# Optimization experiments

Measured on AMD Instinct MI355X. Metric: run time of the kernel, lower is better.

Reference implementation:

```python
import jax, jax.numpy as jnp
import numpy as np

B, S, E, F, C, V = 4, 2048, 100, 64, 8922, 52000

def _conv1d_same(x, w, b, k):
    # x: [B,E,S], w: [F,E,k] -> [B,F,S] with 'same' padding (floor(k/2))
    out = jax.lax.conv_general_dilated(
        x, w, window_strides=(1,), padding=[(k // 2, k // 2)],
        dimension_numbers=('NCH', 'OIH', 'NCH'))
    return out + b[None, :, None]

def setup_inputs() -> dict:
    key = jax.random.key(0)
    ks = jax.random.split(key, 18)
    sc = 0.05
    inp = {
        'x': jax.random.randint(ks[0], (B, S), 0, V),
        'y': (jax.random.uniform(ks[1], (B, C)) < 0.3).astype(jnp.float32),
        'embed': jax.random.normal(ks[2], (V, E), dtype=jnp.float32) * 0.02,
        'w3': jax.random.normal(ks[3], (F, E, 3), dtype=jnp.float32) * sc,
        'b3': jnp.zeros((F,), jnp.float32),
        'w5': jax.random.normal(ks[4], (F, E, 5), dtype=jnp.float32) * sc,
        'b5': jnp.zeros((F,), jnp.float32),
        'w7': jax.random.normal(ks[5], (F, E, 7), dtype=jnp.float32) * sc,
        'b7': jnp.zeros((F,), jnp.float32),
        'w9': jax.random.normal(ks[6], (F, E, 9), dtype=jnp.float32) * sc,
        'b9': jnp.zeros((F,), jnp.float32),
        'U3': jax.random.normal(ks[7], (C, F), dtype=jnp.float32) * sc,
        'U5': jax.random.normal(ks[8], (C, F), dtype=jnp.float32) * sc,
        'U7': jax.random.normal(ks[9], (C, F), dtype=jnp.float32) * sc,
        'U9': jax.random.normal(ks[10], (C, F), dtype=jnp.float32) * sc,
        'Wf': jax.random.normal(ks[11], (C, 4 * F), dtype=jnp.float32) * sc,
        'bf': jnp.zeros((C,), jnp.float32),
    }
    return inp

def reference(x, y, embed, w3, b3, w5, b5, w7, b7, w9, b9, U3, U5, U7, U9, Wf, bf):
    xe = embed[x]                 # [B,S,E] (dropout is identity at inference)
    xt = xe.transpose(0, 2, 1)    # [B,E,S]

    def branch(w, b, U, k):
        h = jnp.tanh(_conv1d_same(xt, w, b, k)).transpose(0, 2, 1)  # [B,S,F]
        scores = jnp.einsum('cf,bsf->bcs', U, h)                    # [B,C,S]
        alpha = jax.nn.softmax(scores, axis=2)
        return jnp.einsum('bcs,bsf->bcf', alpha, h)                 # [B,C,F]

    m = jnp.concatenate([branch(w3, b3, U3, 3), branch(w5, b5, U5, 5),
                         branch(w7, b7, U7, 7), branch(w9, b9, U9, 9)], axis=2)  # [B,C,4F]
    y_hat = jnp.sum(Wf * m, axis=2) + bf                             # [B,C]
    # binary_cross_entropy_with_logits, mean reduction
    loss = jnp.mean(jnp.maximum(y_hat, 0.0) - y_hat * y + jnp.log1p(jnp.exp(-jnp.abs(y_hat))))
    return (y_hat, loss)
```

## Files before the change

kernel.cpp:

```cpp
#include <hip/hip_runtime.h>
#include <hip/hip_bf16.h>

#define B_ 4
#define S_ 2048
#define E_ 100
#define F_ 64
#define C_ 8922
#define V_ 52000

typedef short bf16x8 __attribute__((ext_vector_type(8)));
typedef short s16x4  __attribute__((ext_vector_type(4)));
typedef float f32x4  __attribute__((ext_vector_type(4)));

#define MFMA16(A, B, C) __builtin_amdgcn_mfma_f32_16x16x32_bf16(A, B, C, 0, 0, 0)

__device__ inline short bfb(float x) {
    __hip_bfloat16 h = __float2bfloat16(x);
    return *reinterpret_cast<short*>(&h);
}

__global__ __launch_bounds__(256) void prep_kernel(
    const float* __restrict__ w3, const float* __restrict__ w5,
    const float* __restrict__ w7, const float* __restrict__ w9,
    unsigned short* __restrict__ Wp, float* __restrict__ yhat)
{
    const int gid = blockIdx.x * 256 + threadIdx.x;
    if (gid < B_ * C_) yhat[gid] = 0.f;

    const int j    = gid & 7;
    const int lane = (gid >> 3) & 63;
    const int nt   = (gid >> 9) & 15;
    const int step = gid >> 13;
    const int d    = step >> 2;
    const int ec   = step & 3;
    const int g    = lane >> 4;
    const int lr   = lane & 15;
    const int k    = g * 4 + (j & 3) + ((j >> 2) << 4);
    const int e    = ec * 32 + k;
    const int n    = nt * 16 + lr;
    const int br   = n >> 6;
    const int f    = n & 63;
    const int kb   = 3 + 2 * br;
    const int dp   = d - (3 - br);

    float val = 0.f;
    if (e < E_ && dp >= 0 && dp < kb) {
        const float* w = (br == 0) ? w3 : (br == 1) ? w5 : (br == 2) ? w7 : w9;
        val = w[((size_t)f * E_ + e) * kb + dp];
    }
    Wp[gid] = (unsigned short)bfb(val);
}

__device__ inline void store_h(char* hkB, char* hvB, int b, int br2, int s,
                               int f, float val) {
    const unsigned short u = (unsigned short)bfb(val);
    const size_t cb = ((size_t)(br2 * 4 + b) * 64 + (s >> 5)) * 4096;
    const int sl = s & 31;
    const unsigned ok = ((unsigned)(sl * 128 + f * 2)) ^ ((unsigned)(sl & 7) << 4);
    *(unsigned short*)(hkB + cb + ok) = u;
    const unsigned ov = (unsigned)(((f >> 4) * 512 + ((sl >> 4) & 1) * 256 +
                                    ((sl >> 2) & 3) * 64 + (sl & 3) * 16 +
                                    (f & 15)) * 2);
    *(unsigned short*)(hvB + cb + ov) = u;
}

__global__ __launch_bounds__(256, 1) void conv_mfma_kernel(
    const int* __restrict__ x, const float* __restrict__ embed,
    const unsigned short* __restrict__ Wp,
    const float* __restrict__ b3, const float* __restrict__ b5,
    const float* __restrict__ b7, const float* __restrict__ b9,
    char* __restrict__ hkB, char* __restrict__ hvB)
{
    __shared__ unsigned short xeT[40 * 128];

    const int blk  = blockIdx.x;
    const int b    = blk >> 6;
    const int st   = blk & 63;
    const int s0   = st * 32;
    const int tid  = threadIdx.x;
    const int wave = tid >> 6;
    const int lane = tid & 63;
    const int g    = lane >> 4;
    const int lr   = lane & 15;

    for (int task = tid; task < 640; task += 256) {
        const int row = task >> 4;
        const int o   = task & 15;
        const int s   = s0 - 4 + row;
        float v[8];
        #pragma unroll
        for (int i = 0; i < 8; ++i) v[i] = 0.f;
        if (s >= 0 && s < S_ && o < 13) {
            const int tok = x[b * S_ + s];
            const float* er = embed + (size_t)tok * E_ + o * 8;
            if (o < 12) {
                #pragma unroll
                for (int i = 0; i < 8; ++i) v[i] = er[i];
            } else {
                v[0] = er[0]; v[1] = er[1]; v[2] = er[2]; v[3] = er[3];
            }
        }
        unsigned short u[8];
        #pragma unroll
        for (int i = 0; i < 8; ++i) u[i] = (unsigned short)bfb(v[i]);
        const unsigned xr = ((unsigned)(row & 15)) << 3;
        char* base = (char*)xeT + row * 256;
        *(uint2*)(base + (((unsigned)(o * 16)) ^ xr))     = *(const uint2*)&u[0];
        *(uint2*)(base + (((unsigned)(o * 16 + 8)) ^ xr)) = *(const uint2*)&u[4];
    }
    __syncthreads();

    f32x4 acc[2][4];
    #pragma unroll
    for (int m2 = 0; m2 < 2; ++m2)
        #pragma unroll
        for (int ns = 0; ns < 4; ++ns)
            acc[m2][ns] = (f32x4){0.f, 0.f, 0.f, 0.f};

    const char* xb = (const char*)xeT;
    #pragma unroll
    for (int step = 0; step < 36; ++step) {
        const int d  = step >> 2;
        const int ec = step & 3;

        bf16x8 Af[2];
        #pragma unroll
        for (int m2 = 0; m2 < 2; ++m2) {
            const int row = m2 * 16 + lr + d;
            const unsigned xr = ((unsigned)(row & 15)) << 3;
            const unsigned rb = (unsigned)row * 256;
            const unsigned e0 = (unsigned)(ec * 64 + g * 8);
            const s16x4 lo = *(const s16x4*)(xb + rb + (e0 ^ xr));
            const s16x4 hi = *(const s16x4*)(xb + rb + ((e0 + 32) ^ xr));
            Af[m2] = __builtin_shufflevector(lo, hi, 0, 1, 2, 3, 4, 5, 6, 7);
        }

        bf16x8 Bf[4];
        #pragma unroll
        for (int ns = 0; ns < 4; ++ns)
            Bf[ns] = *(const bf16x8*)(Wp +
                     (((size_t)step * 16 + wave * 4 + ns) * 64 + lane) * 8);

        #pragma unroll
        for (int m2 = 0; m2 < 2; ++m2)
            #pragma unroll
            for (int ns = 0; ns < 4; ++ns)
                acc[m2][ns] = MFMA16(Af[m2], Bf[ns], acc[m2][ns]);
    }

    const float* bias = (wave == 0) ? b3 : (wave == 1) ? b5 : (wave == 2) ? b7 : b9;
    float bia[4];
    #pragma unroll
    for (int ns = 0; ns < 4; ++ns) bia[ns] = bias[ns * 16 + lr];

    #pragma unroll
    for (int m2 = 0; m2 < 2; ++m2)
        #pragma unroll
        for (int ns = 0; ns < 4; ++ns)
            #pragma unroll
            for (int r = 0; r < 4; ++r) {
                const int s = s0 + m2 * 16 + 4 * g + r;
                const int f = ns * 16 + lr;
                store_h(hkB, hvB, b, wave, s, f,
                        tanhf(acc[m2][ns][r] + bia[ns]));
            }
}

#define TRREAD(dst, off) \
    asm volatile("ds_read_b64_tr_b16 %0, %1 offset:" #off \
                 : "=v"(dst) : "v"(vaddr));

typedef const __attribute__((address_space(1))) unsigned int* as1_u32p;
typedef __attribute__((address_space(3))) unsigned int* as3_u32p;

__device__ inline void gl_lds16(const void* g, unsigned lds_off) {
    __builtin_amdgcn_global_load_lds((as1_u32p)(uintptr_t)g,
                                     (as3_u32p)(uintptr_t)lds_off, 16, 0, 0);
}

__global__ __launch_bounds__(256, 2) void attn_mfma_kernel(
    const float* __restrict__ U3, const float* __restrict__ U5,
    const float* __restrict__ U7, const float* __restrict__ U9,
    const char* __restrict__ hkG, const char* __restrict__ hvG,
    const float* __restrict__ Wf, float* __restrict__ yhat)
{
    __shared__ unsigned short Kbuf[2][2048];
    __shared__ unsigned short Vbuf[2][2048];
    __shared__ float ls_lds[4][64];

    const int tid  = threadIdx.x;
    const int wave = tid >> 6;
    const int lane = tid & 63;
    const int g    = lane >> 4;
    const int lr   = lane & 15;

    const int b  = blockIdx.y;
    const int br = blockIdx.z;
    const int c0 = blockIdx.x * 256 + wave * 64;

    const float* __restrict__ U =
        (br == 0) ? U3 : (br == 1) ? U5 : (br == 2) ? U7 : U9;

    bf16x8 Qf[4][2];
    #pragma unroll
    for (int cs = 0; cs < 4; ++cs) {
        int c = c0 + cs * 16 + lr;
        if (c > C_ - 1) c = C_ - 1;
        const float* Uc = U + (size_t)c * F_;
        #pragma unroll
        for (int kh = 0; kh < 2; ++kh) {
            const float4 lo = *(const float4*)(Uc + 32 * kh + 4 * g);
            const float4 hi = *(const float4*)(Uc + 32 * kh + 16 + 4 * g);
            bf16x8 q;
            q[0] = bfb(lo.x); q[1] = bfb(lo.y); q[2] = bfb(lo.z); q[3] = bfb(lo.w);
            q[4] = bfb(hi.x); q[5] = bfb(hi.y); q[6] = bfb(hi.z); q[7] = bfb(hi.w);
            Qf[cs][kh] = q;
        }
    }

    f32x4 acc[4][4];
    #pragma unroll
    for (int cs = 0; cs < 4; ++cs)
        #pragma unroll
        for (int fs = 0; fs < 4; ++fs)
            acc[cs][fs] = (f32x4){0.f, 0.f, 0.f, 0.f};
    float lsum[4] = {0.f, 0.f, 0.f, 0.f};

    const char* hkB = hkG + (size_t)((br * 4 + b) * 64) * 4096;
    const char* hvB = hvG + (size_t)((br * 4 + b) * 64) * 4096;
    const unsigned kL0 = (unsigned)(uintptr_t)&Kbuf[0][0];
    const unsigned vL0 = (unsigned)(uintptr_t)&Vbuf[0][0];

    {
        const size_t go = (size_t)wave * 1024 + (size_t)(lane << 4);
        gl_lds16(hkB + go, kL0 + wave * 1024);
        gl_lds16(hvB + go, vL0 + wave * 1024);
    }
    __syncthreads();

    const unsigned xr = ((unsigned)(lr & 7)) << 4;

    for (int t = 0; t < 64; ++t) {
        const int cur = t & 1;
        if (t < 63) {
            const size_t go = (size_t)(t + 1) * 4096 + (size_t)wave * 1024 +
                              (size_t)(lane << 4);
            const unsigned lo = (unsigned)((cur ^ 1) * 4096 + wave * 1024);
            gl_lds16(hkB + go, kL0 + lo);
            gl_lds16(hvB + go, vL0 + lo);
        }

        const char* Kb = (const char*)Kbuf + cur * 4096;
        bf16x8 Kf[2][2];
        #pragma unroll
        for (int sh = 0; sh < 2; ++sh) {
            const unsigned rowb = (unsigned)((16 * sh + lr) * 128);
            #pragma unroll
            for (int kh = 0; kh < 2; ++kh) {
                const unsigned f1 = ((unsigned)(kh * 64 + g * 8)) ^ xr;
                const unsigned f2 = ((unsigned)(kh * 64 + g * 8 + 32)) ^ xr;
                const s16x4 lo = *(const s16x4*)(Kb + rowb + f1);
                const s16x4 hi = *(const s16x4*)(Kb + rowb + f2);
                Kf[sh][kh] = __builtin_shufflevector(lo, hi, 0, 1, 2, 3, 4, 5, 6, 7);
            }
        }

        const unsigned vaddr = vL0 + (unsigned)(cur * 4096 + g * 128 + lr * 2);
        s16x4 va0, va1, vb0, vb1, vc0, vc1, vd0, vd1;
        TRREAD(va0, 0)    TRREAD(va1, 512)
        TRREAD(vb0, 1024) TRREAD(vb1, 1536)
        TRREAD(vc0, 2048) TRREAD(vc1, 2560)
        TRREAD(vd0, 3072) TRREAD(vd1, 3584)
        asm volatile("s_waitcnt lgkmcnt(0)" ::: "memory");
        __builtin_amdgcn_sched_barrier(0);

        bf16x8 Vf[4];
        Vf[0] = __builtin_shufflevector(va0, va1, 0, 1, 2, 3, 4, 5, 6, 7);
        Vf[1] = __builtin_shufflevector(vb0, vb1, 0, 1, 2, 3, 4, 5, 6, 7);
        Vf[2] = __builtin_shufflevector(vc0, vc1, 0, 1, 2, 3, 4, 5, 6, 7);
        Vf[3] = __builtin_shufflevector(vd0, vd1, 0, 1, 2, 3, 4, 5, 6, 7);

        bf16x8 Pf[4];
        #pragma unroll
        for (int cs = 0; cs < 4; ++cs) {
            f32x4 d0 = (f32x4){0.f, 0.f, 0.f, 0.f};
            f32x4 d1 = (f32x4){0.f, 0.f, 0.f, 0.f};
            d0 = MFMA16(Kf[0][0], Qf[cs][0], d0);
            d0 = MFMA16(Kf[0][1], Qf[cs][1], d0);
            d1 = MFMA16(Kf[1][0], Qf[cs][0], d1);
            d1 = MFMA16(Kf[1][1], Qf[cs][1], d1);
            f32x4 p0, p1;
            #pragma unroll
            for (int r = 0; r < 4; ++r) { p0[r] = __expf(d0[r]); p1[r] = __expf(d1[r]); }
            lsum[cs] += (p0[0] + p0[1] + p0[2] + p0[3]) +
                        (p1[0] + p1[1] + p1[2] + p1[3]);
            bf16x8 pf;
            #pragma unroll
            for (int r = 0; r < 4; ++r) { pf[r] = bfb(p0[r]); pf[4 + r] = bfb(p1[r]); }
            Pf[cs] = pf;
        }

        #pragma unroll
        for (int cs = 0; cs < 4; ++cs)
            #pragma unroll
            for (int fs = 0; fs < 4; ++fs)
                acc[cs][fs] = MFMA16(Pf[cs], Vf[fs], acc[cs][fs]);

        __syncthreads();
    }

    #pragma unroll
    for (int cs = 0; cs < 4; ++cs) {
        lsum[cs] += __shfl_xor(lsum[cs], 16);
        lsum[cs] += __shfl_xor(lsum[cs], 32);
        if (g == 0) ls_lds[wave][cs * 16 + lr] = lsum[cs];
    }
    __syncthreads();

    #pragma unroll
    for (int cs = 0; cs < 4; ++cs) {
        f32x4 linv;
        #pragma unroll
        for (int r = 0; r < 4; ++r)
            linv[r] = 1.f / ls_lds[wave][cs * 16 + 4 * g + r];
        #pragma unroll
        for (int r = 0; r < 4; ++r) {
            const int cc = c0 + cs * 16 + 4 * g + r;
            const int c  = (cc < C_) ? cc : (C_ - 1);
            const float* wrow = Wf + (size_t)c * (4 * F_) + br * F_ + lr;
            float p = 0.f;
            #pragma unroll
            for (int fs = 0; fs < 4; ++fs)
                p += acc[cs][fs][r] * wrow[fs * 16];
            p *= linv[r];
            p += __shfl_xor(p, 1);
            p += __shfl_xor(p, 2);
            p += __shfl_xor(p, 4);
            p += __shfl_xor(p, 8);
            if (lr == 0 && cc < C_)
                atomicAdd(&yhat[(size_t)b * C_ + cc], p);
        }
    }
}

__global__ __launch_bounds__(256) void bce_kernel(
    const float* __restrict__ yhat, const float* __restrict__ bf,
    const float* __restrict__ y, float* __restrict__ out,
    float* __restrict__ partials)
{
    const int p = blockIdx.x * 256 + threadIdx.x;
    float bce = 0.f;
    if (p < B_ * C_) {
        const int c = p % C_;
        const float yh = yhat[p] + bf[c];
        out[p] = yh;
        bce = fmaxf(yh, 0.f) - yh * y[p] + log1pf(expf(-fabsf(yh)));
    }
    __shared__ float red[256];
    red[threadIdx.x] = bce;
    __syncthreads();
    #pragma unroll
    for (int stp = 128; stp > 0; stp >>= 1) {
        if (threadIdx.x < stp) red[threadIdx.x] += red[threadIdx.x + stp];
        __syncthreads();
    }
    if (threadIdx.x == 0) partials[blockIdx.x] = red[0];
}

__global__ __launch_bounds__(256) void loss_kernel(
    const float* __restrict__ partials, int n, float* __restrict__ out_loss)
{
    __shared__ float red[256];
    float v = (threadIdx.x < n) ? partials[threadIdx.x] : 0.f;
    red[threadIdx.x] = v;
    __syncthreads();
    #pragma unroll
    for (int stp = 128; stp > 0; stp >>= 1) {
        if (threadIdx.x < stp) red[threadIdx.x] += red[threadIdx.x + stp];
        __syncthreads();
    }
    if (threadIdx.x == 0) *out_loss = red[0] / (float)(B_ * C_);
}

extern "C" void kernel_launch(void* const* d_in, const int* in_sizes, int n_in,
                              void* d_out, int out_size, void* d_ws, size_t ws_size,
                              hipStream_t stream)
{
    const int*   x     = (const int*)  d_in[0];
    const float* y     = (const float*)d_in[1];
    const float* embed = (const float*)d_in[2];
    const float* w3    = (const float*)d_in[3];
    const float* b3    = (const float*)d_in[4];
    const float* w5    = (const float*)d_in[5];
    const float* b5    = (const float*)d_in[6];
    const float* w7    = (const float*)d_in[7];
    const float* b7    = (const float*)d_in[8];
    const float* w9    = (const float*)d_in[9];
    const float* b9    = (const float*)d_in[10];
    const float* U3    = (const float*)d_in[11];
    const float* U5    = (const float*)d_in[12];
    const float* U7    = (const float*)d_in[13];
    const float* U9    = (const float*)d_in[14];
    const float* Wf    = (const float*)d_in[15];
    const float* bfv   = (const float*)d_in[16];

    char* wsb = (char*)d_ws;
    float*          yhat     = (float*)wsb;
    float*          partials = (float*)(wsb + 142848);
    unsigned short* Wp       = (unsigned short*)(wsb + 143616);
    char*           hkB      = wsb + 737280;
    char*           hvB      = wsb + 737280 + 4194304;
    float*          out      = (float*)d_out;

    prep_kernel<<<1152, 256, 0, stream>>>(w3, w5, w7, w9, Wp, yhat);

    conv_mfma_kernel<<<256, 256, 0, stream>>>(
        x, embed, Wp, b3, b5, b7, b9, hkB, hvB);

    dim3 ag((C_ + 255) / 256, B_, 4);
    attn_mfma_kernel<<<ag, 256, 0, stream>>>(U3, U5, U7, U9, hkB, hvB, Wf, yhat);

    const int nblk = (B_ * C_ + 255) / 256;
    bce_kernel<<<nblk, 256, 0, stream>>>(yhat, bfv, y, out, partials);
    loss_kernel<<<1, 256, 0, stream>>>(partials, nblk, out + B_ * C_);
}
```

Baseline: 257.6 us.

## Widen attention S-tile to 64, use exp2, remap blocks, vectorize conv stores

The attention kernel now handles 64 sequence positions per iteration (32 iterations instead of 64) with double-buffered K/V tiles twice as large. This halves the barriers and loop overhead. Scores are pre-scaled by log2(e) so the exponential can use the native exp2. The K layout changes to a 16-byte swizzle read with single vector loads, and V transposed reads are interleaved with the P·V MFMAs. Blocks use a flat 1D grid remapped so neighbouring blocks share the same branch/batch h data, which helps L2 reuse. The conv epilogue now stages tanh outputs in LDS and writes packed 16-byte stores instead of scattered 2-byte stores. The cost is more LDS and registers per block, which may reduce occupancy.

```diff
diff --git a/kernel.cpp b/kernel.cpp
--- a/kernel.cpp
+++ b/kernel.cpp
@@ -13,6 +13,8 @@
 typedef float f32x4  __attribute__((ext_vector_type(4)));
 
 #define MFMA16(A, B, C) __builtin_amdgcn_mfma_f32_16x16x32_bf16(A, B, C, 0, 0, 0)
+#define LOG2E 1.44269504088896f
+#define EXP2F(x) __builtin_amdgcn_exp2f(x)
 
 __device__ inline short bfb(float x) {
     __hip_bfloat16 h = __float2bfloat16(x);
@@ -51,18 +53,6 @@
     Wp[gid] = (unsigned short)bfb(val);
 }
 
-__device__ inline void store_h(char* hkB, char* hvB, int b, int br2, int s,
-                               int f, float val) {
-    const unsigned short u = (unsigned short)bfb(val);
-    const size_t cb = ((size_t)(br2 * 4 + b) * 64 + (s >> 5)) * 4096;
-    const int sl = s & 31;
-    const unsigned ok = ((unsigned)(sl * 128 + f * 2)) ^ ((unsigned)(sl & 7) << 4);
-    *(unsigned short*)(hkB + cb + ok) = u;
-    const unsigned ov = (unsigned)(((f >> 4) * 512 + ((sl >> 4) & 1) * 256 +
-                                    ((sl >> 2) & 3) * 64 + (sl & 3) * 16 +
-                                    (f & 15)) * 2);
-    *(unsigned short*)(hvB + cb + ov) = u;
-}
 
 __global__ __launch_bounds__(256, 1) void conv_mfma_kernel(
     const int* __restrict__ x, const float* __restrict__ embed,
@@ -72,6 +62,7 @@
     char* __restrict__ hkB, char* __restrict__ hvB)
 {
     __shared__ unsigned short xeT[40 * 128];
+    __shared__ float ep[4][32][68];
 
     const int blk  = blockIdx.x;
     const int b    = blk >> 6;
@@ -158,12 +149,37 @@
         #pragma unroll
         for (int ns = 0; ns < 4; ++ns)
             #pragma unroll
-            for (int r = 0; r < 4; ++r) {
-                const int s = s0 + m2 * 16 + 4 * g + r;
-                const int f = ns * 16 + lr;
-                store_h(hkB, hvB, b, wave, s, f,
-                        tanhf(acc[m2][ns][r] + bia[ns]));
-            }
+            for (int r = 0; r < 4; ++r)
+                ep[wave][m2 * 16 + 4 * g + r][ns * 16 + lr] =
+                    tanhf(acc[m2][ns][r] + bia[ns]);
+    __syncthreads();
+
+    const size_t hbase = (size_t)(wave * 4 + b) * 262144;
+    #pragma unroll
+    for (int it = 0; it < 4; ++it) {
+        const int task = it * 64 + lane;
+        const int sl = task >> 3;
+        const int o  = task & 7;
+        const int s  = s0 + sl;
+        float v[8];
+        *(float4*)&v[0] = *(const float4*)&ep[wave][sl][o * 8];
+        *(float4*)&v[4] = *(const float4*)&ep[wave][sl][o * 8 + 4];
+        unsigned short u[8];
+        #pragma unroll
+        for (int i = 0; i < 8; ++i) u[i] = (unsigned short)bfb(v[i]);
+        uint4 pk;
+        pk.x = (unsigned)u[0] | ((unsigned)u[1] << 16);
+        pk.y = (unsigned)u[2] | ((unsigned)u[3] << 16);
+        pk.z = (unsigned)u[4] | ((unsigned)u[5] << 16);
+        pk.w = (unsigned)u[6] | ((unsigned)u[7] << 16);
+        char* hka = hkB + hbase + (size_t)s * 128 +
+                    (((unsigned)(o * 16)) ^ (((unsigned)(s & 7)) << 4));
+        *(uint4*)hka = pk;
+        char* hva = hvB + hbase + (size_t)(s >> 5) * 4096 + (o >> 1) * 1024 +
+                    ((s >> 4) & 1) * 512 + ((s >> 2) & 3) * 128 +
+                    (s & 3) * 32 + (o & 1) * 16;
+        *(uint4*)hva = pk;
+    }
 }
 
 #define TRREAD(dst, off) \
@@ -184,8 +200,8 @@
     const char* __restrict__ hkG, const char* __restrict__ hvG,
     const float* __restrict__ Wf, float* __restrict__ yhat)
 {
-    __shared__ unsigned short Kbuf[2][2048];
-    __shared__ unsigned short Vbuf[2][2048];
+    __shared__ unsigned short Kbuf[2][4096];
+    __shared__ unsigned short Vbuf[2][4096];
     __shared__ float ls_lds[4][64];
 
     const int tid  = threadIdx.x;
@@ -194,9 +210,13 @@
     const int g    = lane >> 4;
     const int lr   = lane & 15;
 
-    const int b  = blockIdx.y;
-    const int br = blockIdx.z;
-    const int c0 = blockIdx.x * 256 + wave * 64;
+    const int bid = blockIdx.x;
+    const int t2  = bid >> 3;
+    const int grp = (bid & 7) + 8 * (t2 / 35);
+    const int ct  = t2 % 35;
+    const int br  = grp >> 2;
+    const int b   = grp & 3;
+    const int c0  = ct * 256 + wave * 64;
 
     const float* __restrict__ U =
         (br == 0) ? U3 : (br == 1) ? U5 : (br == 2) ? U7 : U9;
@@ -209,11 +229,13 @@
         const float* Uc = U + (size_t)c * F_;
         #pragma unroll
         for (int kh = 0; kh < 2; ++kh) {
-            const float4 lo = *(const float4*)(Uc + 32 * kh + 4 * g);
-            const float4 hi = *(const float4*)(Uc + 32 * kh + 16 + 4 * g);
+            const float4 lo = *(const float4*)(Uc + kh * 32 + g * 8);
+            const float4 hi = *(const float4*)(Uc + kh * 32 + g * 8 + 4);
             bf16x8 q;
-            q[0] = bfb(lo.x); q[1] = bfb(lo.y); q[2] = bfb(lo.z); q[3] = bfb(lo.w);
-            q[4] = bfb(hi.x); q[5] = bfb(hi.y); q[6] = bfb(hi.z); q[7] = bfb(hi.w);
+            q[0] = bfb(lo.x * LOG2E); q[1] = bfb(lo.y * LOG2E);
+            q[2] = bfb(lo.z * LOG2E); q[3] = bfb(lo.w * LOG2E);
+            q[4] = bfb(hi.x * LOG2E); q[5] = bfb(hi.y * LOG2E);
+            q[6] = bfb(hi.z * LOG2E); q[7] = bfb(hi.w * LOG2E);
             Qf[cs][kh] = q;
         }
     }
@@ -226,85 +248,90 @@
             acc[cs][fs] = (f32x4){0.f, 0.f, 0.f, 0.f};
     float lsum[4] = {0.f, 0.f, 0.f, 0.f};
 
-    const char* hkB = hkG + (size_t)((br * 4 + b) * 64) * 4096;
-    const char* hvB = hvG + (size_t)((br * 4 + b) * 64) * 4096;
+    const char* hkB = hkG + (size_t)grp * 262144;
+    const char* hvB = hvG + (size_t)grp * 262144;
     const unsigned kL0 = (unsigned)(uintptr_t)&Kbuf[0][0];
     const unsigned vL0 = (unsigned)(uintptr_t)&Vbuf[0][0];
 
-    {
-        const size_t go = (size_t)wave * 1024 + (size_t)(lane << 4);
-        gl_lds16(hkB + go, kL0 + wave * 1024);
-        gl_lds16(hvB + go, vL0 + wave * 1024);
-    }
-    __syncthreads();
-
-    const unsigned xr = ((unsigned)(lr & 7)) << 4;
-
-    for (int t = 0; t < 64; ++t) {
+#define STAGEKV(chunk, buf) {                                              \
+        const size_t go = (size_t)(chunk) * 8192 + wave * 2048 +           \
+                          (size_t)(lane << 4);                             \
+        const unsigned lo = (unsigned)((buf) * 8192 + wave * 2048);        \
+        gl_lds16(hkB + go,        kL0 + lo);                               \
+        gl_lds16(hkB + go + 1024, kL0 + lo + 1024);                        \
+        gl_lds16(hvB + go,        vL0 + lo);                               \
+        gl_lds16(hvB + go + 1024, vL0 + lo + 1024); }
+
+    STAGEKV(0, 0)
+    __syncthreads();
+
+    const unsigned ksw = ((unsigned)(lr & 7)) << 4;
+
+    for (int t = 0; t < 32; ++t) {
         const int cur = t & 1;
-        if (t < 63) {
-            const size_t go = (size_t)(t + 1) * 4096 + (size_t)wave * 1024 +
-                              (size_t)(lane << 4);
-            const unsigned lo = (unsigned)((cur ^ 1) * 4096 + wave * 1024);
-            gl_lds16(hkB + go, kL0 + lo);
-            gl_lds16(hvB + go, vL0 + lo);
-        }
-
-        const char* Kb = (const char*)Kbuf + cur * 4096;
-        bf16x8 Kf[2][2];
-        #pragma unroll
-        for (int sh = 0; sh < 2; ++sh) {
+        if (t < 31) STAGEKV(t + 1, cur ^ 1)
+
+        const char* Kb = (const char*)Kbuf + cur * 8192;
+        bf16x8 Kf[4][2];
+        #pragma unroll
+        for (int sh = 0; sh < 4; ++sh) {
             const unsigned rowb = (unsigned)((16 * sh + lr) * 128);
             #pragma unroll
-            for (int kh = 0; kh < 2; ++kh) {
-                const unsigned f1 = ((unsigned)(kh * 64 + g * 8)) ^ xr;
-                const unsigned f2 = ((unsigned)(kh * 64 + g * 8 + 32)) ^ xr;
-                const s16x4 lo = *(const s16x4*)(Kb + rowb + f1);
-                const s16x4 hi = *(const s16x4*)(Kb + rowb + f2);
-                Kf[sh][kh] = __builtin_shufflevector(lo, hi, 0, 1, 2, 3, 4, 5, 6, 7);
-            }
-        }
-
-        const unsigned vaddr = vL0 + (unsigned)(cur * 4096 + g * 128 + lr * 2);
-        s16x4 va0, va1, vb0, vb1, vc0, vc1, vd0, vd1;
-        TRREAD(va0, 0)    TRREAD(va1, 512)
-        TRREAD(vb0, 1024) TRREAD(vb1, 1536)
-        TRREAD(vc0, 2048) TRREAD(vc1, 2560)
-        TRREAD(vd0, 3072) TRREAD(vd1, 3584)
-        asm volatile("s_waitcnt lgkmcnt(0)" ::: "memory");
-        __builtin_amdgcn_sched_barrier(0);
-
-        bf16x8 Vf[4];
-        Vf[0] = __builtin_shufflevector(va0, va1, 0, 1, 2, 3, 4, 5, 6, 7);
-        Vf[1] = __builtin_shufflevector(vb0, vb1, 0, 1, 2, 3, 4, 5, 6, 7);
-        Vf[2] = __builtin_shufflevector(vc0, vc1, 0, 1, 2, 3, 4, 5, 6, 7);
-        Vf[3] = __builtin_shufflevector(vd0, vd1, 0, 1, 2, 3, 4, 5, 6, 7);
-
-        bf16x8 Pf[4];
+            for (int kh = 0; kh < 2; ++kh)
+                Kf[sh][kh] = *(const bf16x8*)(
+                    Kb + rowb + (((unsigned)(kh * 64 + g * 16)) ^ ksw));
+        }
+
+        bf16x8 Pf[4][2];
         #pragma unroll
         for (int cs = 0; cs < 4; ++cs) {
-            f32x4 d0 = (f32x4){0.f, 0.f, 0.f, 0.f};
-            f32x4 d1 = (f32x4){0.f, 0.f, 0.f, 0.f};
+            f32x4 d0 = (f32x4){0.f,0.f,0.f,0.f}, d1 = d0, d2 = d0, d3 = d0;
             d0 = MFMA16(Kf[0][0], Qf[cs][0], d0);
             d0 = MFMA16(Kf[0][1], Qf[cs][1], d0);
             d1 = MFMA16(Kf[1][0], Qf[cs][0], d1);
             d1 = MFMA16(Kf[1][1], Qf[cs][1], d1);
-            f32x4 p0, p1;
-            #pragma unroll
-            for (int r = 0; r < 4; ++r) { p0[r] = __expf(d0[r]); p1[r] = __expf(d1[r]); }
-            lsum[cs] += (p0[0] + p0[1] + p0[2] + p0[3]) +
-                        (p1[0] + p1[1] + p1[2] + p1[3]);
-            bf16x8 pf;
-            #pragma unroll
-            for (int r = 0; r < 4; ++r) { pf[r] = bfb(p0[r]); pf[4 + r] = bfb(p1[r]); }
-            Pf[cs] = pf;
-        }
-
-        #pragma unroll
-        for (int cs = 0; cs < 4; ++cs)
-            #pragma unroll
-            for (int fs = 0; fs < 4; ++fs)
-                acc[cs][fs] = MFMA16(Pf[cs], Vf[fs], acc[cs][fs]);
+            d2 = MFMA16(Kf[2][0], Qf[cs][0], d2);
+            d2 = MFMA16(Kf[2][1], Qf[cs][1], d2);
+            d3 = MFMA16(Kf[3][0], Qf[cs][0], d3);
+            d3 = MFMA16(Kf[3][1], Qf[cs][1], d3);
+            float p[16];
+            #pragma unroll
+            for (int r = 0; r < 4; ++r) {
+                p[r]      = EXP2F(d0[r]);
+                p[4 + r]  = EXP2F(d1[r]);
+                p[8 + r]  = EXP2F(d2[r]);
+                p[12 + r] = EXP2F(d3[r]);
+            }
+            float sm = 0.f;
+            #pragma unroll
+            for (int r = 0; r < 16; ++r) sm += p[r];
+            lsum[cs] += sm;
+            bf16x8 pf0, pf1;
+            #pragma unroll
+            for (int r = 0; r < 8; ++r) { pf0[r] = bfb(p[r]); pf1[r] = bfb(p[8 + r]); }
+            Pf[cs][0] = pf0;
+            Pf[cs][1] = pf1;
+        }
+
+        const unsigned vaddr = vL0 + (unsigned)(cur * 8192 + g * 128 + lr * 2);
+#define PVBLK(fs, O0, O1, O2, O3)                                          \
+        {                                                                  \
+            s16x4 a0, a1, b0, b1;                                          \
+            TRREAD(a0, O0) TRREAD(a1, O1) TRREAD(b0, O2) TRREAD(b1, O3)    \
+            asm volatile("s_waitcnt lgkmcnt(0)" ::: "memory");             \
+            __builtin_amdgcn_sched_barrier(0);                             \
+            const bf16x8 V0 = __builtin_shufflevector(a0, a1, 0,1,2,3,4,5,6,7); \
+            const bf16x8 V1 = __builtin_shufflevector(b0, b1, 0,1,2,3,4,5,6,7); \
+            _Pragma("unroll")                                              \
+            for (int cs = 0; cs < 4; ++cs) {                               \
+                acc[cs][fs] = MFMA16(Pf[cs][0], V0, acc[cs][fs]);          \
+                acc[cs][fs] = MFMA16(Pf[cs][1], V1, acc[cs][fs]);          \
+            }                                                              \
+        }
+        PVBLK(0,    0,  512, 4096, 4608)
+        PVBLK(1, 1024, 1536, 5120, 5632)
+        PVBLK(2, 2048, 2560, 6144, 6656)
+        PVBLK(3, 3072, 3584, 7168, 7680)
 
         __syncthreads();
     }
@@ -417,8 +444,7 @@
     conv_mfma_kernel<<<256, 256, 0, stream>>>(
         x, embed, Wp, b3, b5, b7, b9, hkB, hvB);
 
-    dim3 ag((C_ + 255) / 256, B_, 4);
-    attn_mfma_kernel<<<ag, 256, 0, stream>>>(U3, U5, U7, U9, hkB, hvB, Wf, yhat);
+    attn_mfma_kernel<<<560, 256, 0, stream>>>(U3, U5, U7, U9, hkB, hvB, Wf, yhat);
 
     const int nblk = (B_ * C_ + 255) / 256;
     bce_kernel<<<nblk, 256, 0, stream>>>(yhat, bfv, y, out, partials);
```

Result: faster. 235.7 us (-8.5%).
